# Optimization experiments

Measured on AMD Instinct MI355X. Metric: run time of the kernel, lower is better.

## Reference

```python
import jax, jax.numpy as jnp
import numpy as np
import math

P = 2
TAU = 1.0
USE_POW = False
ALIGN_W = 1.0
ENTROPY_W = 1.0
EPS = 1e-12


def _pairwise_l2(z):
    # torch.cdist(z, z, p=2): sqrt of squared distances via GEMM decomposition
    sq = jnp.sum(z * z, axis=-1)  # [N]
    d2 = sq[:, None] + sq[None, :] - 2.0 * (z @ z.T)  # [N, N]
    d = jnp.sqrt(jnp.maximum(d2, 0.0))
    return jnp.maximum(d, EPS)  # clamp_min(eps)


def setup_inputs() -> dict:
    key = jax.random.key(0)
    k0, k1 = jax.random.split(key)
    v0 = jax.random.normal(k0, (8192, 256), dtype=jnp.float32)
    v1 = jax.random.normal(k1, (8192, 256), dtype=jnp.float32)
    return {"v0": v0, "v1": v1}


def reference(v0, v1):
    views = [v0, v1]
    n = v0.shape[0]

    # Alignment term: mean Lp distance between matched rows, one pair (0,1)
    diff = v0 - v1
    align = jnp.sqrt(jnp.sum(diff * diff, axis=-1)).mean()  # p=2 norm per row

    # Entropy term: masked logsumexp over within-view pairwise distances
    log_num_neg = math.log(n - 1)
    eye = jnp.eye(n, dtype=bool)
    entropy = jnp.float32(0.0)
    for z in views:
        dist = _pairwise_l2(z)  # [N, N]
        logits = jnp.where(eye, -jnp.inf, -dist / TAU)
        lme = jax.nn.logsumexp(logits, axis=1) - log_num_neg  # [N]
        entropy = entropy + lme.mean()
    entropy = entropy / len(views)

    return ALIGN_W * align + ENTROPY_W * entropy
```

## Files before the change

kernel.cpp:

```cpp
#include <hip/hip_runtime.h>
#include <math.h>


#define D_DIM 256
#define NB 64
#define NSEG 1056
#define S_Q 26.0f
#define LOG2E2 2.0813689810f
#define LP 65

typedef int i32x4 __attribute__((ext_vector_type(4)));
typedef unsigned int u32;
#define AS1 __attribute__((address_space(1)))
#define AS3 __attribute__((address_space(3)))

__device__ inline void load_lds16(const void* g, void* l) {
  __builtin_amdgcn_global_load_lds((const AS1 u32*)g, (AS3 u32*)l, 16, 0, 0);
}

__device__ inline int q8(float x) {
  return __float2int_rn(fminf(fmaxf(x * S_Q, -127.0f), 127.0f));
}
__device__ inline u32 q8x4(const float4 f) {
  return (u32)(q8(f.x) & 255) | ((u32)(q8(f.y) & 255) << 8) |
         ((u32)(q8(f.z) & 255) << 16) | ((u32)(q8(f.w) & 255) << 24);
}

__device__ inline int Gfun(int M) {
  const int m = M >> 1;
  return (M & 1) ? (m + 1) * (m + 1) : m * (m + 1);
}

__global__ __launch_bounds__(256) void prep(
    const float* __restrict__ v0, const float* __restrict__ v1,
    unsigned char* __restrict__ ph0, unsigned char* __restrict__ ph1,
    float* __restrict__ sq0, float* __restrict__ sq1,
    float* __restrict__ S0, float* __restrict__ S1,
    float* __restrict__ align_part,
    double* __restrict__ totals, int* __restrict__ ticket) {
  __shared__ float4 l0[16 * LP], l1[16 * LP];
  __shared__ float red0[4][16], red1[4][16], red2[4][16];
  const int R = blockIdx.x;
  const int t = threadIdx.x;

  if (R == 0 && t == 0) { totals[0] = 0.0; totals[1] = 0.0; ticket[0] = 0; }

  #pragma unroll
  for (int p = 0; p < 4; ++p) {
    const int slot = t + p * 256;
    const int r = slot >> 6, col = slot & 63;
    const size_t g = (size_t)(R * 16 + r) * 64 + col;
    l0[r * LP + col] = ((const float4*)v0)[g];
    l1[r * LP + col] = ((const float4*)v1)[g];
  }
  __syncthreads();

  {
    const int rr = t & 15, c = t >> 4;
    const int s = c >> 2, q = c & 3;
    const int li = rr * LP + c * 4;
    uint4 u0, u1;
    u0.x = q8x4(l0[li + 0]); u0.y = q8x4(l0[li + 1]);
    u0.z = q8x4(l0[li + 2]); u0.w = q8x4(l0[li + 3]);
    u1.x = q8x4(l1[li + 0]); u1.y = q8x4(l1[li + 1]);
    u1.z = q8x4(l1[li + 2]); u1.w = q8x4(l1[li + 3]);
    const size_t dst = (size_t)(R * 4 + s) * 64 + q * 16 + rr;
    ((uint4*)ph0)[dst] = u0;
    ((uint4*)ph1)[dst] = u1;
  }

  {
    const int rr = t & 15;
    const int base = rr * LP + (t >> 4) * 4;
    float s0p = 0.f, s1p = 0.f, s2p = 0.f;
    #pragma unroll
    for (int c = 0; c < 4; ++c) {
      const float4 a = l0[base + c], b = l1[base + c];
      s0p += a.x * a.x + a.y * a.y + a.z * a.z + a.w * a.w;
      s1p += b.x * b.x + b.y * b.y + b.z * b.z + b.w * b.w;
      const float dx = a.x - b.x, dy = a.y - b.y, dz = a.z - b.z, dw = a.w - b.w;
      s2p += dx * dx + dy * dy + dz * dz + dw * dw;
    }
    s0p += __shfl_xor(s0p, 16, 64); s0p += __shfl_xor(s0p, 32, 64);
    s1p += __shfl_xor(s1p, 16, 64); s1p += __shfl_xor(s1p, 32, 64);
    s2p += __shfl_xor(s2p, 16, 64); s2p += __shfl_xor(s2p, 32, 64);
    const int w = t >> 6, lane = t & 63;
    if (lane < 16) { red0[w][lane] = s0p; red1[w][lane] = s1p; red2[w][lane] = s2p; }
  }
  __syncthreads();
  if (t < 16) {
    const int row = R * 16 + t;
    const float a0 = red0[0][t] + red0[1][t] + red0[2][t] + red0[3][t];
    const float a1 = red1[0][t] + red1[1][t] + red1[2][t] + red1[3][t];
    const float a2 = red2[0][t] + red2[1][t] + red2[2][t] + red2[3][t];
    sq0[row] = a0 * LOG2E2;
    sq1[row] = a1 * LOG2E2;
    align_part[row] = sqrtf(a2);
    S0[row] = 0.0f;
    S1[row] = 0.0f;
  }
}

__global__ __launch_bounds__(256) void entropy_tile(
    const unsigned char* __restrict__ ph0, const unsigned char* __restrict__ ph1,
    const float* __restrict__ sq0, const float* __restrict__ sq1,
    float* __restrict__ S0, float* __restrict__ S1) {
  const unsigned char* __restrict__ ph = blockIdx.y ? ph1 : ph0;
  const float* __restrict__ sq = blockIdx.y ? sq1 : sq0;
  float* __restrict__ S        = blockIdx.y ? S1 : S0;

  const int lin = blockIdx.x;
  int bi = 0;
  while (NSEG - Gfun(64 - (bi + 1)) <= lin) ++bi;
  const int q = lin - (NSEG - Gfun(64 - bi));
  const int bj0 = bi + 2 * q;

  __shared__ __align__(16) char smem[32768];
  float* swp = (float*)smem;

  const int t = threadIdx.x, lane = t & 63, w = t >> 6;
  const int wi = w >> 1, wj = w & 1;
  const int quad = lane >> 4, l15 = lane & 15;
  const int i0 = bi * 128;

  #pragma unroll
  for (int r8 = 0; r8 < 8; ++r8) {
    const int seg = w * 8 + r8;
    const unsigned char* src = ph + (size_t)bi * 32768 + seg * 1024 + lane * 16;
    load_lds16(src, smem + seg * 1024);
  }

  const i32x4* __restrict__ phv = (const i32x4*)ph;
  const i32x4* smemv = (const i32x4*)smem;
  const float K2 = 2.0f * LOG2E2 / (S_Q * S_Q);

  const int bjA = bj0;
  const bool diagA = (bj0 == bi);
  const bool haveB = (bj0 + 1 < NB);
  const int j0A = bjA * 128;

  float prow[4][4];
  #pragma unroll
  for (int m = 0; m < 4; ++m)
    #pragma unroll
    for (int r = 0; r < 4; ++r) prow[m][r] = 0.f;

  i32x4 bF[4][4];
  float sjlA[4], sjlB[4];
  float csumA[4] = {0.f, 0.f, 0.f, 0.f}, csumB[4] = {0.f, 0.f, 0.f, 0.f};
  i32x4 accA[4], accB[4];
  float siA[4], siB[4];

  auto loadB = [&](const int bj) {
    const int baseB = ((bj * 8 + wj * 4) * 4) * 64 + lane;
    #pragma unroll
    for (int s = 0; s < 4; ++s)
      #pragma unroll
      for (int n = 0; n < 4; ++n)
        bF[s][n] = phv[baseB + (n * 4 + s) * 64];
  };
  auto loadSj = [&](const int bj, float* sjl) {
    #pragma unroll
    for (int n = 0; n < 4; ++n) sjl[n] = sq[bj * 128 + wj * 64 + n * 16 + l15];
  };

  loadSj(bjA, sjlA);
  loadB(bjA);
  __syncthreads();

  auto compute = [&](i32x4* acc, float* si, const int m) {
    #pragma unroll
    for (int r = 0; r < 4; ++r)
      si[r] = sq[i0 + wi * 64 + m * 16 + quad * 4 + r];
    #pragma unroll
    for (int n = 0; n < 4; ++n) acc[n] = (i32x4){0, 0, 0, 0};
    #pragma unroll
    for (int s = 0; s < 4; ++s) {
      const i32x4 ah = smemv[(size_t)((wi * 4 + m) * 4 + s) * 64 + lane];
      #pragma unroll
      for (int n = 0; n < 4; ++n)
        acc[n] = __builtin_amdgcn_mfma_i32_16x16x64_i8(ah, bF[s][n], acc[n], 0, 0, 0);
    }
  };

  auto epilogue = [&](const i32x4* acc, const float* si, const int m,
                      const float* sjl, float* csum, const int j0,
                      const bool diag_t) {
    #pragma unroll
    for (int r = 0; r < 4; ++r) {
      const int gi = i0 + wi * 64 + m * 16 + quad * 4 + r;
      float p = 0.f;
      #pragma unroll
      for (int n = 0; n < 4; ++n) {
        const float d2 = fmaf(-K2, (float)acc[n][r], si[r] + sjl[n]);
        float e = __builtin_amdgcn_exp2f(-__builtin_amdgcn_sqrtf(d2));
        if (diag_t && gi == j0 + wj * 64 + n * 16 + l15) e = 0.f;
        p += e;
        csum[n] += e;
      }
      prow[m][r] += p;
    }
  };

  auto flushCsum = [&](const float* csum, const int j0) {
    #pragma unroll
    for (int n = 0; n < 4; ++n) {
      float c2 = csum[n];
      c2 += __shfl_xor(c2, 16, 64);
      c2 += __shfl_xor(c2, 32, 64);
      if (quad == 0) atomicAdd(&S[j0 + wj * 64 + n * 16 + l15], c2);
    }
  };

  compute(accA, siA, 0);
  compute(accB, siB, 1);
  epilogue(accA, siA, 0, sjlA, csumA, j0A, diagA);
  compute(accA, siA, 2);
  epilogue(accB, siB, 1, sjlA, csumA, j0A, diagA);
  compute(accB, siB, 3);
  if (haveB) { loadSj(bjA + 1, sjlB); loadB(bjA + 1); }
  epilogue(accA, siA, 2, sjlA, csumA, j0A, diagA);
  epilogue(accB, siB, 3, sjlA, csumA, j0A, diagA);
  if (!diagA) flushCsum(csumA, j0A);

  if (haveB) {
    const int j0B = (bjA + 1) * 128;
    compute(accA, siA, 0);
    compute(accB, siB, 1);
    epilogue(accA, siA, 0, sjlB, csumB, j0B, false);
    compute(accA, siA, 2);
    epilogue(accB, siB, 1, sjlB, csumB, j0B, false);
    compute(accB, siB, 3);
    epilogue(accA, siA, 2, sjlB, csumB, j0B, false);
    epilogue(accB, siB, 3, sjlB, csumB, j0B, false);
    flushCsum(csumB, j0B);
  }

  __syncthreads();

  const int wbase = w * 1088;
  #pragma unroll
  for (int m = 0; m < 4; ++m)
    #pragma unroll
    for (int r = 0; r < 4; ++r)
      swp[wbase + (m * 16 + quad * 4 + r) * 17 + l15] = prow[m][r];
  float rs = 0.f;
  #pragma unroll
  for (int j = 0; j < 16; ++j) rs += swp[wbase + lane * 17 + j];
  atomicAdd(&S[i0 + wi * 64 + lane], rs);
}

__global__ __launch_bounds__(256) void finalize_fused(
    const float* __restrict__ S0, const float* __restrict__ S1,
    const float* __restrict__ align_part,
    double* __restrict__ totals, int* __restrict__ ticket,
    float* __restrict__ out, int n) {
  __shared__ float shl[4], sha[4];
  const int t = threadIdx.x, lane = t & 63, w = t >> 6;
  const int idx = blockIdx.x * 256 + t;
  float lg = __logf(S0[idx]) + __logf(S1[idx]);
  float al = align_part[idx];
  #pragma unroll
  for (int o = 1; o < 64; o <<= 1) {
    lg += __shfl_xor(lg, o, 64);
    al += __shfl_xor(al, o, 64);
  }
  if (lane == 0) { shl[w] = lg; sha[w] = al; }
  __syncthreads();
  if (t == 0) {
    const double pl = (double)(shl[0] + shl[1] + shl[2] + shl[3]);
    const double pa = (double)(sha[0] + sha[1] + sha[2] + sha[3]);
    atomicAdd(&totals[0], pl);
    atomicAdd(&totals[1], pa);
    __threadfence();
    const int old = atomicAdd(ticket, 1);
    if (old == (int)gridDim.x - 1) {
      const double lgt = atomicAdd(&totals[0], 0.0);
      const double alt = atomicAdd(&totals[1], 0.0);
      const double align = alt / (double)n;
      const double entropy = 0.5 * lgt / (double)n - log((double)(n - 1));
      out[0] = (float)(align + entropy);
    }
  }
}

extern "C" void kernel_launch(void* const* d_in, const int* in_sizes, int n_in,
                              void* d_out, int out_size, void* d_ws, size_t ws_size,
                              hipStream_t stream) {
  const float* v0 = (const float*)d_in[0];
  const float* v1 = (const float*)d_in[1];
  float* out = (float*)d_out;
  const int n = in_sizes[0] / D_DIM;

  float* ws         = (float*)d_ws;
  float* sq0        = ws;
  float* sq1        = ws + n;
  float* S0         = ws + 2 * n;
  float* S1         = ws + 3 * n;
  float* align_part = ws + 4 * n;
  double* totals    = (double*)(ws + 5 * n);
  int* ticket       = (int*)(ws + 5 * n + 4);
  unsigned char* ph0 = (unsigned char*)(ws + 5 * n + 64);
  unsigned char* ph1 = ph0 + (size_t)n * D_DIM;

  prep<<<n / 16, 256, 0, stream>>>(v0, v1, ph0, ph1, sq0, sq1, S0, S1,
                                   align_part, totals, ticket);

  dim3 grid(NSEG, 2);
  entropy_tile<<<grid, 256, 0, stream>>>(ph0, ph1, sq0, sq1, S0, S1);

  finalize_fused<<<n / 256, 256, 0, stream>>>(S0, S1, align_part, totals,
                                              ticket, out, n);
}
```

Measured before the change: 134.8 us.

## Process up to four column tiles per block in entropy kernel

Each block of the triangular entropy kernel now covers up to four 128-wide column tiles per row tile instead of two, which roughly halves the grid (NSEG 1056 to 544). The block-to-tile mapping becomes a general loop over tiles, so the row-tile LDS load and the row-sum atomics are amortised over more work. The explicit prefetch of the next tile's B fragments during the current tile's epilogue is removed, so load latency is now left to the compiler, and fewer blocks may leave CUs underfilled.

Result: faster. 111.2 us (-17.5%).

```diff
diff --git a/kernel.cpp b/kernel.cpp
--- a/kernel.cpp
+++ b/kernel.cpp
@@ -4,7 +4,7 @@
 
 #define D_DIM 256
 #define NB 64
-#define NSEG 1056
+#define NSEG 544
 #define S_Q 26.0f
 #define LOG2E2 2.0813689810f
 #define LP 65
@@ -26,9 +26,9 @@
          ((u32)(q8(f.z) & 255) << 16) | ((u32)(q8(f.w) & 255) << 24);
 }
 
-__device__ inline int Gfun(int M) {
-  const int m = M >> 1;
-  return (M & 1) ? (m + 1) * (m + 1) : m * (m + 1);
+__device__ inline int G4fun(int M) {
+  const int m = M >> 2, r = M & 3;
+  return 2 * m * (m + 1) + r * (m + 1);
 }
 
 __global__ __launch_bounds__(256) void prep(
@@ -111,9 +111,10 @@
 
   const int lin = blockIdx.x;
   int bi = 0;
-  while (NSEG - Gfun(64 - (bi + 1)) <= lin) ++bi;
-  const int q = lin - (NSEG - Gfun(64 - bi));
-  const int bj0 = bi + 2 * q;
+  while (NSEG - G4fun(64 - (bi + 1)) <= lin) ++bi;
+  const int q = lin - (NSEG - G4fun(64 - bi));
+  const int bj0 = bi + 4 * q;
+  const int jend = (bj0 + 3 < NB - 1) ? bj0 + 3 : NB - 1;
 
   __shared__ __align__(16) char smem[32768];
   float* swp = (float*)smem;
@@ -129,112 +130,93 @@
     const unsigned char* src = ph + (size_t)bi * 32768 + seg * 1024 + lane * 16;
     load_lds16(src, smem + seg * 1024);
   }
+  __syncthreads();
 
   const i32x4* __restrict__ phv = (const i32x4*)ph;
   const i32x4* smemv = (const i32x4*)smem;
   const float K2 = 2.0f * LOG2E2 / (S_Q * S_Q);
 
-  const int bjA = bj0;
-  const bool diagA = (bj0 == bi);
-  const bool haveB = (bj0 + 1 < NB);
-  const int j0A = bjA * 128;
-
   float prow[4][4];
   #pragma unroll
   for (int m = 0; m < 4; ++m)
     #pragma unroll
     for (int r = 0; r < 4; ++r) prow[m][r] = 0.f;
 
-  i32x4 bF[4][4];
-  float sjlA[4], sjlB[4];
-  float csumA[4] = {0.f, 0.f, 0.f, 0.f}, csumB[4] = {0.f, 0.f, 0.f, 0.f};
-  i32x4 accA[4], accB[4];
-  float siA[4], siB[4];
-
-  auto loadB = [&](const int bj) {
+  auto do_tile = [&](const int bj, const bool diag_t) {
+    const int j0 = bj * 128;
     const int baseB = ((bj * 8 + wj * 4) * 4) * 64 + lane;
+
+    float sjl[4];
+    #pragma unroll
+    for (int n = 0; n < 4; ++n) sjl[n] = sq[j0 + wj * 64 + n * 16 + l15];
+
+    i32x4 bF[4][4];
     #pragma unroll
     for (int s = 0; s < 4; ++s)
       #pragma unroll
       for (int n = 0; n < 4; ++n)
         bF[s][n] = phv[baseB + (n * 4 + s) * 64];
-  };
-  auto loadSj = [&](const int bj, float* sjl) {
-    #pragma unroll
-    for (int n = 0; n < 4; ++n) sjl[n] = sq[bj * 128 + wj * 64 + n * 16 + l15];
-  };
-
-  loadSj(bjA, sjlA);
-  loadB(bjA);
-  __syncthreads();
-
-  auto compute = [&](i32x4* acc, float* si, const int m) {
-    #pragma unroll
-    for (int r = 0; r < 4; ++r)
-      si[r] = sq[i0 + wi * 64 + m * 16 + quad * 4 + r];
-    #pragma unroll
-    for (int n = 0; n < 4; ++n) acc[n] = (i32x4){0, 0, 0, 0};
-    #pragma unroll
-    for (int s = 0; s < 4; ++s) {
-      const i32x4 ah = smemv[(size_t)((wi * 4 + m) * 4 + s) * 64 + lane];
-      #pragma unroll
-      for (int n = 0; n < 4; ++n)
-        acc[n] = __builtin_amdgcn_mfma_i32_16x16x64_i8(ah, bF[s][n], acc[n], 0, 0, 0);
+
+    float csum[4] = {0.f, 0.f, 0.f, 0.f};
+
+    i32x4 accA[4], accB[4];
+    float siA[4], siB[4];
+
+    auto compute = [&](i32x4* acc, float* si, const int m) {
+      #pragma unroll
+      for (int r = 0; r < 4; ++r)
+        si[r] = sq[i0 + wi * 64 + m * 16 + quad * 4 + r];
+      #pragma unroll
+      for (int n = 0; n < 4; ++n) acc[n] = (i32x4){0, 0, 0, 0};
+      #pragma unroll
+      for (int s = 0; s < 4; ++s) {
+        const i32x4 ah = smemv[(size_t)((wi * 4 + m) * 4 + s) * 64 + lane];
+        #pragma unroll
+        for (int n = 0; n < 4; ++n)
+          acc[n] = __builtin_amdgcn_mfma_i32_16x16x64_i8(ah, bF[s][n], acc[n], 0, 0, 0);
+      }
+    };
+
+    auto epilogue = [&](const i32x4* acc, const float* si, const int m) {
+      #pragma unroll
+      for (int r = 0; r < 4; ++r) {
+        const int gi = i0 + wi * 64 + m * 16 + quad * 4 + r;
+        float p = 0.f;
+        #pragma unroll
+        for (int n = 0; n < 4; ++n) {
+          const float d2 = fmaf(-K2, (float)acc[n][r], si[r] + sjl[n]);
+          float e = __builtin_amdgcn_exp2f(-__builtin_amdgcn_sqrtf(d2));
+          if (diag_t && gi == j0 + wj * 64 + n * 16 + l15) e = 0.f;
+          p += e;
+          csum[n] += e;
+        }
+        prow[m][r] += p;
+      }
+    };
+
+    compute(accA, siA, 0);
+    compute(accB, siB, 1);
+    epilogue(accA, siA, 0);
+    compute(accA, siA, 2);
+    epilogue(accB, siB, 1);
+    compute(accB, siB, 3);
+    epilogue(accA, siA, 2);
+    epilogue(accB, siB, 3);
+
+    if (!diag_t) {
+      #pragma unroll
+      for (int n = 0; n < 4; ++n) {
+        float c2 = csum[n];
+        c2 += __shfl_xor(c2, 16, 64);
+        c2 += __shfl_xor(c2, 32, 64);
+        if (quad == 0) atomicAdd(&S[j0 + wj * 64 + n * 16 + l15], c2);
+      }
     }
   };
 
-  auto epilogue = [&](const i32x4* acc, const float* si, const int m,
-                      const float* sjl, float* csum, const int j0,
-                      const bool diag_t) {
-    #pragma unroll
-    for (int r = 0; r < 4; ++r) {
-      const int gi = i0 + wi * 64 + m * 16 + quad * 4 + r;
-      float p = 0.f;
-      #pragma unroll
-      for (int n = 0; n < 4; ++n) {
-        const float d2 = fmaf(-K2, (float)acc[n][r], si[r] + sjl[n]);
-        float e = __builtin_amdgcn_exp2f(-__builtin_amdgcn_sqrtf(d2));
-        if (diag_t && gi == j0 + wj * 64 + n * 16 + l15) e = 0.f;
-        p += e;
-        csum[n] += e;
-      }
-      prow[m][r] += p;
-    }
-  };
-
-  auto flushCsum = [&](const float* csum, const int j0) {
-    #pragma unroll
-    for (int n = 0; n < 4; ++n) {
-      float c2 = csum[n];
-      c2 += __shfl_xor(c2, 16, 64);
-      c2 += __shfl_xor(c2, 32, 64);
-      if (quad == 0) atomicAdd(&S[j0 + wj * 64 + n * 16 + l15], c2);
-    }
-  };
-
-  compute(accA, siA, 0);
-  compute(accB, siB, 1);
-  epilogue(accA, siA, 0, sjlA, csumA, j0A, diagA);
-  compute(accA, siA, 2);
-  epilogue(accB, siB, 1, sjlA, csumA, j0A, diagA);
-  compute(accB, siB, 3);
-  if (haveB) { loadSj(bjA + 1, sjlB); loadB(bjA + 1); }
-  epilogue(accA, siA, 2, sjlA, csumA, j0A, diagA);
-  epilogue(accB, siB, 3, sjlA, csumA, j0A, diagA);
-  if (!diagA) flushCsum(csumA, j0A);
-
-  if (haveB) {
-    const int j0B = (bjA + 1) * 128;
-    compute(accA, siA, 0);
-    compute(accB, siB, 1);
-    epilogue(accA, siA, 0, sjlB, csumB, j0B, false);
-    compute(accA, siA, 2);
-    epilogue(accB, siB, 1, sjlB, csumB, j0B, false);
-    compute(accB, siB, 3);
-    epilogue(accA, siA, 2, sjlB, csumB, j0B, false);
-    epilogue(accB, siB, 3, sjlB, csumB, j0B, false);
-    flushCsum(csumB, j0B);
-  }
+  int bjs = bj0;
+  if (bj0 == bi) { do_tile(bi, true); bjs = bi + 1; }
+  for (int bj = bjs; bj <= jend; ++bj) do_tile(bj, false);
 
   __syncthreads();
 
```
